# Kernel optimization log

Hardware: AMD Instinct MI355X
Metric: run time of the kernel (lower is better)

The kernel has to match this reference:

```python
import jax, jax.numpy as jnp
import numpy as np

B, C, D, H, W = 1, 32, 48, 96, 192


def setup_inputs() -> dict:
    key = jax.random.key(0)
    ks = jax.random.split(key, 5)
    x = jax.random.normal(ks[0], (B, C, D, H, W), dtype=jnp.float32)
    gs = []
    for i in range(4):
        g = jax.random.uniform(ks[i + 1], (B, C, 5, H, W), dtype=jnp.float32)
        # GANet normalizes the 5 aggregation weights to sum to 1 per pixel
        g = g / jnp.sum(g, axis=2, keepdims=True)
        gs.append(g)
    return {"input": x, "g0": gs[0], "g1": gs[1], "g2": gs[2], "g3": gs[3]}


def _sga_dir(cost, g, axis, reverse):
    """Semi-global aggregation along one direction.

    cost: (B,C,D,H,W); g: (B,C,5,H,W). axis=4 scans along width, axis=3 along
    height; reverse flips the scan direction. Recurrence per step p:
      A(p,d) = w0*C(p,d) + w1*A(p-1,d) + w2*A(p-1,d-1) + w3*A(p-1,d+1)
               + w4*max_d' A(p-1,d')
    with A = C at the first position and d+-1 edge-clamped.
    """
    c = jnp.moveaxis(cost, axis, 0)  # (L, B, C, D, R)
    w = jnp.moveaxis(g, axis, 0)     # (L, B, C, 5, R)
    if reverse:
        c = c[::-1]
        w = w[::-1]

    def step(A, xs):
        cs, ws = xs  # cs: (B,C,D,R); ws: (B,C,5,R)
        w0, w1, w2, w3, w4 = (ws[:, :, k][:, :, None] for k in range(5))
        dm1 = jnp.concatenate([A[:, :, :1], A[:, :, :-1]], axis=2)  # d-1 (clamped)
        dp1 = jnp.concatenate([A[:, :, 1:], A[:, :, -1:]], axis=2)  # d+1 (clamped)
        mx = jnp.max(A, axis=2, keepdims=True)                      # max over d
        A_new = w0 * cs + w1 * A + w2 * dm1 + w3 * dp1 + w4 * mx
        return A_new, A_new

    A0 = c[0]
    _, outs = jax.lax.scan(step, A0, (c[1:], w[1:]))
    full = jnp.concatenate([A0[None], outs], axis=0)
    if reverse:
        full = full[::-1]
    return jnp.moveaxis(full, 0, axis)


def reference(input, g0, g1, g2, g3):
    a0 = _sga_dir(input, g0, 4, False)  # left -> right
    a1 = _sga_dir(input, g1, 4, True)   # right -> left
    a2 = _sga_dir(input, g2, 3, False)  # top -> bottom
    a3 = _sga_dir(input, g3, 3, True)   # bottom -> top
    # GANet selects the max over the 4 directions instead of summing
    return jnp.maximum(jnp.maximum(a0, a1), jnp.maximum(a2, a3))
```

## Files before the change

kernel.cpp:

```cpp
#include <hip/hip_runtime.h>

constexpr int Cc = 32;
constexpr int Dd = 48;
constexpr int Hh = 96;
constexpr int Ww = 192;
constexpr int TW = 16;
constexpr int NT = Ww / TW;
constexpr float NEGBIG = -3.402823466e+38f;

template <int CTRL, int RM>
__device__ __forceinline__ float dppmov(float v) {
    int i = __builtin_bit_cast(int, v);
    int r = __builtin_amdgcn_update_dpp(i, i, CTRL, RM, 0xF, false);
    return __builtin_bit_cast(float, r);
}

__device__ __forceinline__ float rdlane(float v, int idx) {
    int r = __builtin_amdgcn_readlane(__builtin_bit_cast(int, v), idx);
    return __builtin_bit_cast(float, r);
}

__device__ __forceinline__ unsigned f2h(float v) {
    return (unsigned)__builtin_bit_cast(unsigned short, (_Float16)v);
}
__device__ __forceinline__ float h2f(unsigned short u) {
    return (float)__builtin_bit_cast(_Float16, u);
}

__device__ __forceinline__ float wave_max48(float v) {
    v = fmaxf(v, dppmov<0x111, 0xF>(v));
    v = fmaxf(v, dppmov<0x112, 0xF>(v));
    v = fmaxf(v, dppmov<0x114, 0xF>(v));
    v = fmaxf(v, dppmov<0x118, 0xF>(v));
    v = fmaxf(v, dppmov<0x142, 0x2>(v));
    v = fmaxf(v, dppmov<0x143, 0x4>(v));
    return rdlane(v, 47);
}

__device__ __forceinline__ float sga_step(float A, float cs, float g0v, float g1v, float g2v,
                                          float g3v, float g4v, bool is47, bool first) {
    float dm1 = dppmov<0x138, 0xF>(A);
    float dp1 = dppmov<0x130, 0xF>(A);
    dp1 = is47 ? A : dp1;
    float mx = wave_max48(A);
    float r = g0v * cs + g1v * A + g2v * dm1 + g3v * dp1 + g4v * mx;
    return first ? cs : r;
}

template <bool WS>
__global__ __launch_bounds__(64, 4) void sga_w4(const float* __restrict__ x,
                                                const float* __restrict__ ga,
                                                const float* __restrict__ gb,
                                                float* __restrict__ out,
                                                const unsigned* __restrict__ ws) {
    __shared__ unsigned sstash[64][Dd];
    __shared__ float xo[Dd][TW + 1];

    const int bid = blockIdx.x;
    const int c = bid / Hh;
    const int h = bid - c * Hh;
    const int lane = threadIdx.x;
    const size_t HW = (size_t)Hh * Ww;

    const float* xrow = x + (size_t)c * Dd * HW + (size_t)h * Ww;
    const float* garow = ga + (size_t)c * 5 * HW + (size_t)h * Ww;
    const float* gbrow = gb + (size_t)c * 5 * HW + (size_t)h * Ww;
    float* orow = out + (size_t)c * Dd * HW + (size_t)h * Ww;
    const size_t wsrow = ((size_t)c * Hh + h) * Dd;

    const int dl = (lane < Dd) ? lane : (Dd - 1);
    const bool is47 = (lane == Dd - 1);

    int srow[3], scol[3];
#pragma unroll
    for (int i = 0; i < 3; ++i) {
        const int e4 = lane + i * 64;
        srow[i] = e4 >> 2;
        scol[i] = (e4 & 3) * 4;
    }
    const int gk = lane >> 4;
    const int gwi = lane & 15;

    float4 pre[3];
    float gA, g4r, gAn = 0.f, g4n = 0.f;
    unsigned tr[8];
    unsigned sv0[8], sv1[8], sv2[8], sv3[8];

    {
#pragma unroll
        for (int i = 0; i < 3; ++i)
            pre[i] = *reinterpret_cast<const float4*>(xrow + (size_t)srow[i] * HW + scol[i]);
        gA = garow[(size_t)gk * HW + gwi];
        g4r = garow[(size_t)4 * HW + gwi];
#pragma unroll
        for (int i = 0; i < 3; ++i) {
            xo[srow[i]][scol[i] + 0] = pre[i].x;
            xo[srow[i]][scol[i] + 1] = pre[i].y;
            xo[srow[i]][scol[i] + 2] = pre[i].z;
            xo[srow[i]][scol[i] + 3] = pre[i].w;
        }
    }

    float A = NEGBIG;

    for (int t = 0; t < NT; ++t) {
        if (t + 1 < NT) {
            const int wn = (t + 1) * TW;
#pragma unroll
            for (int i = 0; i < 3; ++i)
                pre[i] = *reinterpret_cast<const float4*>(xrow + (size_t)srow[i] * HW + wn + scol[i]);
            gAn = garow[(size_t)gk * HW + wn + gwi];
            g4n = garow[(size_t)4 * HW + wn + gwi];
        }
#pragma unroll
        for (int wk = 0; wk < TW; ++wk) {
            const float g0v = rdlane(gA, wk);
            const float g1v = rdlane(gA, 16 + wk);
            const float g2v = rdlane(gA, 32 + wk);
            const float g3v = rdlane(gA, 48 + wk);
            const float g4v = rdlane(g4r, wk);
            const float cs = xo[dl][wk];
            A = sga_step(A, cs, g0v, g1v, g2v, g3v, g4v, is47, (t == 0 && wk == 0));
            const unsigned hu = f2h(A);
            if ((wk & 1) == 0) tr[wk >> 1] = hu;
            else tr[wk >> 1] |= hu << 16;
        }
        if (t < 8) {
            if (lane < Dd) {
#pragma unroll
                for (int r = 0; r < 8; ++r) sstash[t * 8 + r][lane] = tr[r];
            }
        } else if (t == 8) {
#pragma unroll
            for (int r = 0; r < 8; ++r) sv0[r] = tr[r];
        } else if (t == 9) {
#pragma unroll
            for (int r = 0; r < 8; ++r) sv1[r] = tr[r];
        } else if (t == 10) {
#pragma unroll
            for (int r = 0; r < 8; ++r) sv2[r] = tr[r];
        } else {
#pragma unroll
            for (int r = 0; r < 8; ++r) sv3[r] = tr[r];
        }
        if (t + 1 < NT) {
#pragma unroll
            for (int i = 0; i < 3; ++i) {
                xo[srow[i]][scol[i] + 0] = pre[i].x;
                xo[srow[i]][scol[i] + 1] = pre[i].y;
                xo[srow[i]][scol[i] + 2] = pre[i].z;
                xo[srow[i]][scol[i] + 3] = pre[i].w;
            }
            gA = gAn;
            g4r = g4n;
        }
    }

    A = NEGBIG;
    unsigned wsc[6], wsn[6];
    {
        const int w0 = (NT - 1) * TW;
        gA = gbrow[(size_t)gk * HW + w0 + gwi];
        g4r = gbrow[(size_t)4 * HW + w0 + gwi];
        if constexpr (WS) {
#pragma unroll
            for (int i = 0; i < 3; ++i) {
                const size_t wb = (wsrow + srow[i]) * 96 + (w0 >> 1) + (scol[i] >> 1);
                wsc[2 * i] = ws[wb];
                wsc[2 * i + 1] = ws[wb + 1];
            }
        }
    }
    for (int t = NT - 1; t >= 0; --t) {
        const int w0 = t * TW;
        if (t > 0) {
            const int wn = w0 - TW;
#pragma unroll
            for (int i = 0; i < 3; ++i)
                pre[i] = *reinterpret_cast<const float4*>(xrow + (size_t)srow[i] * HW + wn + scol[i]);
            gAn = gbrow[(size_t)gk * HW + wn + gwi];
            g4n = gbrow[(size_t)4 * HW + wn + gwi];
            if constexpr (WS) {
#pragma unroll
                for (int i = 0; i < 3; ++i) {
                    const size_t wb = (wsrow + srow[i]) * 96 + (wn >> 1) + (scol[i] >> 1);
                    wsn[2 * i] = ws[wb];
                    wsn[2 * i + 1] = ws[wb + 1];
                }
            }
        }
        unsigned rr[8];
        if (t < 8) {
#pragma unroll
            for (int r = 0; r < 8; ++r) rr[r] = sstash[t * 8 + r][dl];
        } else if (t == 8) {
#pragma unroll
            for (int r = 0; r < 8; ++r) rr[r] = sv0[r];
        } else if (t == 9) {
#pragma unroll
            for (int r = 0; r < 8; ++r) rr[r] = sv1[r];
        } else if (t == 10) {
#pragma unroll
            for (int r = 0; r < 8; ++r) rr[r] = sv2[r];
        } else {
#pragma unroll
            for (int r = 0; r < 8; ++r) rr[r] = sv3[r];
        }
#pragma unroll
        for (int wk = TW - 1; wk >= 0; --wk) {
            const float g0v = rdlane(gA, wk);
            const float g1v = rdlane(gA, 16 + wk);
            const float g2v = rdlane(gA, 32 + wk);
            const float g3v = rdlane(gA, 48 + wk);
            const float g4v = rdlane(g4r, wk);
            const float cs = xo[dl][wk];
            A = sga_step(A, cs, g0v, g1v, g2v, g3v, g4v, is47, (t == NT - 1 && wk == TW - 1));
            const unsigned u = rr[wk >> 1];
            const float a0 = h2f((unsigned short)((wk & 1) ? (u >> 16) : (u & 0xffffu)));
            if (lane < Dd) xo[lane][wk] = fmaxf(A, a0);
        }
#pragma unroll
        for (int i = 0; i < 3; ++i) {
            float4 v;
            v.x = xo[srow[i]][scol[i] + 0];
            v.y = xo[srow[i]][scol[i] + 1];
            v.z = xo[srow[i]][scol[i] + 2];
            v.w = xo[srow[i]][scol[i] + 3];
            if constexpr (WS) {
                v.x = fmaxf(v.x, h2f((unsigned short)(wsc[2 * i] & 0xffffu)));
                v.y = fmaxf(v.y, h2f((unsigned short)(wsc[2 * i] >> 16)));
                v.z = fmaxf(v.z, h2f((unsigned short)(wsc[2 * i + 1] & 0xffffu)));
                v.w = fmaxf(v.w, h2f((unsigned short)(wsc[2 * i + 1] >> 16)));
            }
            *reinterpret_cast<float4*>(orow + (size_t)srow[i] * HW + w0 + scol[i]) = v;
        }
        if (t > 0) {
#pragma unroll
            for (int i = 0; i < 3; ++i) {
                xo[srow[i]][scol[i] + 0] = pre[i].x;
                xo[srow[i]][scol[i] + 1] = pre[i].y;
                xo[srow[i]][scol[i] + 2] = pre[i].z;
                xo[srow[i]][scol[i] + 3] = pre[i].w;
            }
            gA = gAn;
            g4r = g4n;
            if constexpr (WS) {
#pragma unroll
                for (int i = 0; i < 6; ++i) wsc[i] = wsn[i];
            }
        }
    }
}

constexpr int WT2 = 4;
constexpr int KH2 = 2;
constexpr int NP2 = Hh / KH2;
constexpr int HALF2 = NP2 / 2;

template <bool WS>
__global__ __launch_bounds__(512, 2) void sga_h4(const float* __restrict__ x,
                                                 const float* __restrict__ gf,
                                                 const float* __restrict__ gr,
                                                 float* __restrict__ out,
                                                 unsigned* __restrict__ ws) {
    __shared__ unsigned short stash[WT2][2][Hh / 2][Dd];
    __shared__ float xs[2][2][KH2][Dd][WT2 + 1];
    __shared__ unsigned short osb[2][2][KH2][Dd][6];
    __shared__ float gs[2][2][KH2][WT2][8];

    const int xcd = blockIdx.x & 7;
    const int within = blockIdx.x >> 3;
    const int L = xcd * 192 + within;
    const int quad = L >> 2, sub = L & 3;
    const int c = quad / 12;
    const int wq = quad % 12;
    const int w0 = wq * 16 + sub * 4;

    const int tid = threadIdx.x;
    const int lane = tid & 63;
    const int wv = tid >> 6;
    const int col = wv >> 1;
    const int dir = wv & 1;
    const size_t HW = (size_t)Hh * Ww;

    const float* xb = x + (size_t)c * Dd * HW;
    const float* gfb = gf + (size_t)c * 5 * HW;
    const float* grb = gr + (size_t)c * 5 * HW;
    float* ob = out + (size_t)c * Dd * HW;

    const int dl = (lane < Dd) ? lane : (Dd - 1);
    const bool is47 = (lane == Dd - 1);

    int w_[2], d_[2], hp_[2], cu_[2];
    bool val_[2];
    size_t xoff_[2];
#pragma unroll
    for (int j = 0; j < 2; ++j) {
        int idx = tid + j * 512;
        val_[j] = idx < 768;
        if (idx >= 768) idx = 767;
        w_[j] = idx & 3;
        const int tt = idx >> 2;
        d_[j] = tt % Dd;
        const int t2 = tt / Dd;
        hp_[j] = t2 & 1;
        cu_[j] = t2 >> 1;
        xoff_[j] = (size_t)d_[j] * HW + (w0 + w_[j]);
    }
    const int gw_ = tid & 3;
    const int gk_ = (tid >> 2) % 5;
    const int ghc = (tid >> 2) / 5;
    const int ghp_ = ghc & 1;
    const int gcu_ = ghc >> 1;
    const bool gst = tid < 80;
    const int fwu = tid & 1;
    const int fd = (tid >> 1) % Dd;
    const int fr = (tid >> 1) / Dd;
    const int fhp = fr & 1;
    const int fcu = fr >> 1;
    const bool fval = tid < 384;

    auto hofs = [&](int cur, int P, int hp) -> int {
        const int p = P * KH2 + hp;
        return cur ? (Hh - 1 - p) : p;
    };

    float xr_[2], grg = 0.f;
    float orr[2][2];

    {
#pragma unroll
        for (int j = 0; j < 2; ++j)
            if (val_[j]) xr_[j] = xb[xoff_[j] + (size_t)hofs(cu_[j], 0, hp_[j]) * Ww];
        if (gst) {
            const float* gp = gcu_ ? grb : gfb;
            grg = gp[(size_t)gk_ * HW + (size_t)hofs(gcu_, 0, ghp_) * Ww + (w0 + gw_)];
        }
#pragma unroll
        for (int j = 0; j < 2; ++j)
            if (val_[j]) xs[0][cu_[j]][hp_[j]][d_[j]][w_[j]] = xr_[j];
        if (gst) gs[0][gcu_][ghp_][gw_][gk_] = grg;
    }
    __syncthreads();

    float A = NEGBIG;

#pragma unroll 2
    for (int p = 0; p < NP2; ++p) {
        const int pb = p & 1;

        if (p + 1 < NP2) {
#pragma unroll
            for (int j = 0; j < 2; ++j)
                if (val_[j]) xr_[j] = xb[xoff_[j] + (size_t)hofs(cu_[j], p + 1, hp_[j]) * Ww];
            if (gst) {
                const float* gp = gcu_ ? grb : gfb;
                grg = gp[(size_t)gk_ * HW + (size_t)hofs(gcu_, p + 1, ghp_) * Ww + (w0 + gw_)];
            }
        }
        if constexpr (!WS) {
            if (p >= HALF2) {
#pragma unroll
                for (int j = 0; j < 2; ++j)
                    if (val_[j]) orr[pb][j] = ob[xoff_[j] + (size_t)hofs(cu_[j], p, hp_[j]) * Ww];
            }
        }

#pragma unroll
        for (int hp = 0; hp < KH2; ++hp) {
            const int q = p * KH2 + hp;
            const float cs = xs[pb][dir][hp][dl][col];
            const float* gbase = &gs[pb][dir][hp][col][0];
            const float4 g03 = *reinterpret_cast<const float4*>(gbase);
            const float g4 = gbase[4];
            A = sga_step(A, cs, g03.x, g03.y, g03.z, g03.w, g4, is47, q == 0);
            if (q < Hh / 2) {
                if (lane < Dd) stash[col][dir][q][lane] = (unsigned short)f2h(A);
            } else {
                const float s = h2f(stash[col][dir ^ 1][Hh - 1 - q][dl]);
                const float o = fmaxf(A, s);
                if (lane < Dd) osb[pb][dir][hp][lane][col] = (unsigned short)f2h(o);
            }
        }

        if (p > HALF2) {
            if constexpr (WS) {
                if (fval) {
                    const unsigned* op = reinterpret_cast<const unsigned*>(&osb[pb ^ 1][fcu][fhp][fd][0]);
                    const unsigned v = op[fwu];
                    const int hh = hofs(fcu, p - 1, fhp);
                    ws[(((size_t)c * Hh + hh) * Dd + fd) * 96 + (w0 >> 1) + fwu] = v;
                }
            } else {
#pragma unroll
                for (int j = 0; j < 2; ++j) {
                    if (val_[j]) {
                        const float v = fmaxf(h2f(osb[pb ^ 1][cu_[j]][hp_[j]][d_[j]][w_[j]]),
                                              orr[pb ^ 1][j]);
                        ob[xoff_[j] + (size_t)hofs(cu_[j], p - 1, hp_[j]) * Ww] = v;
                    }
                }
            }
        }

        if (p + 1 < NP2) {
#pragma unroll
            for (int j = 0; j < 2; ++j)
                if (val_[j]) xs[pb ^ 1][cu_[j]][hp_[j]][d_[j]][w_[j]] = xr_[j];
            if (gst) gs[pb ^ 1][gcu_][ghp_][gw_][gk_] = grg;
        }
        __syncthreads();
    }

    if constexpr (WS) {
        if (fval) {
            const unsigned* op = reinterpret_cast<const unsigned*>(&osb[1][fcu][fhp][fd][0]);
            const unsigned v = op[fwu];
            const int hh = hofs(fcu, NP2 - 1, fhp);
            ws[(((size_t)c * Hh + hh) * Dd + fd) * 96 + (w0 >> 1) + fwu] = v;
        }
    } else {
#pragma unroll
        for (int j = 0; j < 2; ++j) {
            if (val_[j]) {
                const float v = fmaxf(h2f(osb[1][cu_[j]][hp_[j]][d_[j]][w_[j]]), orr[1][j]);
                ob[xoff_[j] + (size_t)hofs(cu_[j], NP2 - 1, hp_[j]) * Ww] = v;
            }
        }
    }
}

extern "C" void kernel_launch(void* const* d_in, const int* in_sizes, int n_in,
                              void* d_out, int out_size, void* d_ws, size_t ws_size,
                              hipStream_t stream) {
    const float* x  = (const float*)d_in[0];
    const float* g0 = (const float*)d_in[1];
    const float* g1 = (const float*)d_in[2];
    const float* g2 = (const float*)d_in[3];
    const float* g3 = (const float*)d_in[4];
    float* out = (float*)d_out;

    const size_t WSNEED = (size_t)Cc * Hh * Dd * Ww * 2;
    if (ws_size >= WSNEED) {
        sga_h4<true><<<Cc * (Ww / WT2), 512, 0, stream>>>(x, g2, g3, out, (unsigned*)d_ws);
        sga_w4<true><<<Cc * Hh, 64, 0, stream>>>(x, g0, g1, out, (const unsigned*)d_ws);
    } else {
        sga_w4<false><<<Cc * Hh, 64, 0, stream>>>(x, g0, g1, out, nullptr);
        sga_h4<false><<<Cc * (Ww / WT2), 512, 0, stream>>>(x, g2, g3, out, nullptr);
    }
}
```

Before: 289.8 us.

## Replace block-cooperative vertical scan with per-thread register scan over disparity

```diff
diff --git a/kernel.cpp b/kernel.cpp
--- a/kernel.cpp
+++ b/kernel.cpp
@@ -242,191 +242,127 @@
                 xo[srow[i]][scol[i] + 2] = pre[i].z;
                 xo[srow[i]][scol[i] + 3] = pre[i].w;
             }
+#pragma unroll
+            for (int i = 0; i < 6; ++i) wsc[i] = wsn[i];
             gA = gAn;
             g4r = g4n;
-            if constexpr (WS) {
-#pragma unroll
-                for (int i = 0; i < 6; ++i) wsc[i] = wsn[i];
-            }
-        }
-    }
-}
-
-constexpr int WT2 = 4;
-constexpr int KH2 = 2;
-constexpr int NP2 = Hh / KH2;
-constexpr int HALF2 = NP2 / 2;
-
-template <bool WS>
-__global__ __launch_bounds__(512, 2) void sga_h4(const float* __restrict__ x,
-                                                 const float* __restrict__ gf,
-                                                 const float* __restrict__ gr,
-                                                 float* __restrict__ out,
-                                                 unsigned* __restrict__ ws) {
-    __shared__ unsigned short stash[WT2][2][Hh / 2][Dd];
-    __shared__ float xs[2][2][KH2][Dd][WT2 + 1];
-    __shared__ unsigned short osb[2][2][KH2][Dd][6];
-    __shared__ float gs[2][2][KH2][WT2][8];
-
-    const int xcd = blockIdx.x & 7;
-    const int within = blockIdx.x >> 3;
-    const int L = xcd * 192 + within;
-    const int quad = L >> 2, sub = L & 3;
-    const int c = quad / 12;
-    const int wq = quad % 12;
-    const int w0 = wq * 16 + sub * 4;
-
-    const int tid = threadIdx.x;
-    const int lane = tid & 63;
-    const int wv = tid >> 6;
-    const int col = wv >> 1;
-    const int dir = wv & 1;
+        }
+    }
+}
+
+template <bool REV, int MODE>
+__global__ __launch_bounds__(64) void sga_hreg(const float* __restrict__ x,
+                                               const float* __restrict__ g,
+                                               unsigned short* __restrict__ ws,
+                                               float* __restrict__ out) {
+    const int c = blockIdx.x / 3;
+    const int w = (blockIdx.x % 3) * 64 + threadIdx.x;
     const size_t HW = (size_t)Hh * Ww;
 
     const float* xb = x + (size_t)c * Dd * HW;
-    const float* gfb = gf + (size_t)c * 5 * HW;
-    const float* grb = gr + (size_t)c * 5 * HW;
+    const float* gb = g + (size_t)c * 5 * HW;
+    unsigned short* wsb = ws + (size_t)c * Hh * Dd * Ww;
     float* ob = out + (size_t)c * Dd * HW;
 
-    const int dl = (lane < Dd) ? lane : (Dd - 1);
-    const bool is47 = (lane == Dd - 1);
-
-    int w_[2], d_[2], hp_[2], cu_[2];
-    bool val_[2];
-    size_t xoff_[2];
-#pragma unroll
-    for (int j = 0; j < 2; ++j) {
-        int idx = tid + j * 512;
-        val_[j] = idx < 768;
-        if (idx >= 768) idx = 767;
-        w_[j] = idx & 3;
-        const int tt = idx >> 2;
-        d_[j] = tt % Dd;
-        const int t2 = tt / Dd;
-        hp_[j] = t2 & 1;
-        cu_[j] = t2 >> 1;
-        xoff_[j] = (size_t)d_[j] * HW + (w0 + w_[j]);
-    }
-    const int gw_ = tid & 3;
-    const int gk_ = (tid >> 2) % 5;
-    const int ghc = (tid >> 2) / 5;
-    const int ghp_ = ghc & 1;
-    const int gcu_ = ghc >> 1;
-    const bool gst = tid < 80;
-    const int fwu = tid & 1;
-    const int fd = (tid >> 1) % Dd;
-    const int fr = (tid >> 1) / Dd;
-    const int fhp = fr & 1;
-    const int fcu = fr >> 1;
-    const bool fval = tid < 384;
-
-    auto hofs = [&](int cur, int P, int hp) -> int {
-        const int p = P * KH2 + hp;
-        return cur ? (Hh - 1 - p) : p;
-    };
-
-    float xr_[2], grg = 0.f;
-    float orr[2][2];
+    auto hof = [](int p) { return REV ? (Hh - 1 - p) : p; };
+
+    float A[Dd], xr[Dd], gr[5], gn[5];
+    unsigned short hl[Dd];
+    float wl[Dd];
 
     {
-#pragma unroll
-        for (int j = 0; j < 2; ++j)
-            if (val_[j]) xr_[j] = xb[xoff_[j] + (size_t)hofs(cu_[j], 0, hp_[j]) * Ww];
-        if (gst) {
-            const float* gp = gcu_ ? grb : gfb;
-            grg = gp[(size_t)gk_ * HW + (size_t)hofs(gcu_, 0, ghp_) * Ww + (w0 + gw_)];
-        }
-#pragma unroll
-        for (int j = 0; j < 2; ++j)
-            if (val_[j]) xs[0][cu_[j]][hp_[j]][d_[j]][w_[j]] = xr_[j];
-        if (gst) gs[0][gcu_][ghp_][gw_][gk_] = grg;
-    }
-    __syncthreads();
-
-    float A = NEGBIG;
-
-#pragma unroll 2
-    for (int p = 0; p < NP2; ++p) {
-        const int pb = p & 1;
-
-        if (p + 1 < NP2) {
-#pragma unroll
-            for (int j = 0; j < 2; ++j)
-                if (val_[j]) xr_[j] = xb[xoff_[j] + (size_t)hofs(cu_[j], p + 1, hp_[j]) * Ww];
-            if (gst) {
-                const float* gp = gcu_ ? grb : gfb;
-                grg = gp[(size_t)gk_ * HW + (size_t)hofs(gcu_, p + 1, ghp_) * Ww + (w0 + gw_)];
-            }
-        }
-        if constexpr (!WS) {
-            if (p >= HALF2) {
-#pragma unroll
-                for (int j = 0; j < 2; ++j)
-                    if (val_[j]) orr[pb][j] = ob[xoff_[j] + (size_t)hofs(cu_[j], p, hp_[j]) * Ww];
-            }
-        }
-
-#pragma unroll
-        for (int hp = 0; hp < KH2; ++hp) {
-            const int q = p * KH2 + hp;
-            const float cs = xs[pb][dir][hp][dl][col];
-            const float* gbase = &gs[pb][dir][hp][col][0];
-            const float4 g03 = *reinterpret_cast<const float4*>(gbase);
-            const float g4 = gbase[4];
-            A = sga_step(A, cs, g03.x, g03.y, g03.z, g03.w, g4, is47, q == 0);
-            if (q < Hh / 2) {
-                if (lane < Dd) stash[col][dir][q][lane] = (unsigned short)f2h(A);
-            } else {
-                const float s = h2f(stash[col][dir ^ 1][Hh - 1 - q][dl]);
-                const float o = fmaxf(A, s);
-                if (lane < Dd) osb[pb][dir][hp][lane][col] = (unsigned short)f2h(o);
-            }
-        }
-
-        if (p > HALF2) {
-            if constexpr (WS) {
-                if (fval) {
-                    const unsigned* op = reinterpret_cast<const unsigned*>(&osb[pb ^ 1][fcu][fhp][fd][0]);
-                    const unsigned v = op[fwu];
-                    const int hh = hofs(fcu, p - 1, fhp);
-                    ws[(((size_t)c * Hh + hh) * Dd + fd) * 96 + (w0 >> 1) + fwu] = v;
-                }
-            } else {
-#pragma unroll
-                for (int j = 0; j < 2; ++j) {
-                    if (val_[j]) {
-                        const float v = fmaxf(h2f(osb[pb ^ 1][cu_[j]][hp_[j]][d_[j]][w_[j]]),
-                                              orr[pb ^ 1][j]);
-                        ob[xoff_[j] + (size_t)hofs(cu_[j], p - 1, hp_[j]) * Ww] = v;
-                    }
-                }
-            }
-        }
-
-        if (p + 1 < NP2) {
-#pragma unroll
-            for (int j = 0; j < 2; ++j)
-                if (val_[j]) xs[pb ^ 1][cu_[j]][hp_[j]][d_[j]][w_[j]] = xr_[j];
-            if (gst) gs[pb ^ 1][gcu_][ghp_][gw_][gk_] = grg;
-        }
-        __syncthreads();
-    }
-
-    if constexpr (WS) {
-        if (fval) {
-            const unsigned* op = reinterpret_cast<const unsigned*>(&osb[1][fcu][fhp][fd][0]);
-            const unsigned v = op[fwu];
-            const int hh = hofs(fcu, NP2 - 1, fhp);
-            ws[(((size_t)c * Hh + hh) * Dd + fd) * 96 + (w0 >> 1) + fwu] = v;
-        }
-    } else {
-#pragma unroll
-        for (int j = 0; j < 2; ++j) {
-            if (val_[j]) {
-                const float v = fmaxf(h2f(osb[1][cu_[j]][hp_[j]][d_[j]][w_[j]]), orr[1][j]);
-                ob[xoff_[j] + (size_t)hofs(cu_[j], NP2 - 1, hp_[j]) * Ww] = v;
-            }
-        }
+        const int h0 = hof(0);
+#pragma unroll
+        for (int d = 0; d < Dd; ++d) xr[d] = xb[(size_t)d * HW + (size_t)h0 * Ww + w];
+        if (MODE == 1) {
+#pragma unroll
+            for (int d = 0; d < Dd; ++d) hl[d] = wsb[((size_t)h0 * Dd + d) * Ww + w];
+        } else if (MODE == 2) {
+#pragma unroll
+            for (int d = 0; d < Dd; ++d) wl[d] = ob[(size_t)d * HW + (size_t)h0 * Ww + w];
+        }
+        const int h1 = hof(1);
+#pragma unroll
+        for (int k = 0; k < 5; ++k) gr[k] = gb[(size_t)k * HW + (size_t)h1 * Ww + w];
+    }
+
+    {
+        const int h0 = hof(0);
+        const int h1 = hof(1);
+#pragma unroll
+        for (int d = 0; d < Dd; ++d) {
+            A[d] = xr[d];
+            if (MODE == 0)
+                wsb[((size_t)h0 * Dd + d) * Ww + w] = (unsigned short)f2h(A[d]);
+            xr[d] = xb[(size_t)d * HW + (size_t)h1 * Ww + w];
+        }
+    }
+
+    for (int p = 1; p < Hh; ++p) {
+        const int h = hof(p);
+        const int hn = hof(p + 1);
+        const bool notlast = (p + 1 < Hh);
+
+        if (notlast) {
+#pragma unroll
+            for (int k = 0; k < 5; ++k) gn[k] = gb[(size_t)k * HW + (size_t)hn * Ww + w];
+        }
+
+        if (MODE == 1) {
+            const int hm = hof(p - 1);
+#pragma unroll
+            for (int d = 0; d < Dd; ++d) {
+                const float m = fmaxf(A[d], h2f(hl[d]));
+                wsb[((size_t)hm * Dd + d) * Ww + w] = (unsigned short)f2h(m);
+                hl[d] = wsb[((size_t)h * Dd + d) * Ww + w];
+            }
+        } else if (MODE == 2) {
+            const int hm = hof(p - 1);
+#pragma unroll
+            for (int d = 0; d < Dd; ++d) {
+                ob[(size_t)d * HW + (size_t)hm * Ww + w] = fmaxf(A[d], wl[d]);
+                wl[d] = ob[(size_t)d * HW + (size_t)h * Ww + w];
+            }
+        }
+
+        float t0[24];
+#pragma unroll
+        for (int i = 0; i < 24; ++i) t0[i] = fmaxf(A[2 * i], A[2 * i + 1]);
+#pragma unroll
+        for (int i = 0; i < 12; ++i) t0[i] = fmaxf(t0[i], t0[i + 12]);
+#pragma unroll
+        for (int i = 0; i < 6; ++i) t0[i] = fmaxf(t0[i], t0[i + 6]);
+#pragma unroll
+        for (int i = 0; i < 3; ++i) t0[i] = fmaxf(t0[i], t0[i + 3]);
+        const float M = fmaxf(t0[0], fmaxf(t0[1], t0[2]));
+
+        float pm = A[0];
+#pragma unroll
+        for (int d = 0; d < Dd; ++d) {
+            const float cur = A[d];
+            const float np = (d < Dd - 1) ? A[d + 1] : cur;
+            A[d] = gr[0] * xr[d] + gr[1] * cur + gr[2] * pm + gr[3] * np + gr[4] * M;
+            pm = cur;
+            if (MODE == 0)
+                wsb[((size_t)h * Dd + d) * Ww + w] = (unsigned short)f2h(A[d]);
+            if (notlast) xr[d] = xb[(size_t)d * HW + (size_t)hn * Ww + w];
+        }
+#pragma unroll
+        for (int k = 0; k < 5; ++k) gr[k] = gn[k];
+    }
+
+    if (MODE == 1) {
+        const int hm = hof(Hh - 1);
+#pragma unroll
+        for (int d = 0; d < Dd; ++d) {
+            const float m = fmaxf(A[d], h2f(hl[d]));
+            wsb[((size_t)hm * Dd + d) * Ww + w] = (unsigned short)f2h(m);
+        }
+    } else if (MODE == 2) {
+        const int hm = hof(Hh - 1);
+#pragma unroll
+        for (int d = 0; d < Dd; ++d)
+            ob[(size_t)d * HW + (size_t)hm * Ww + w] = fmaxf(A[d], wl[d]);
     }
 }
 
@@ -442,10 +378,12 @@
 
     const size_t WSNEED = (size_t)Cc * Hh * Dd * Ww * 2;
     if (ws_size >= WSNEED) {
-        sga_h4<true><<<Cc * (Ww / WT2), 512, 0, stream>>>(x, g2, g3, out, (unsigned*)d_ws);
+        sga_hreg<false, 0><<<Cc * 3, 64, 0, stream>>>(x, g2, (unsigned short*)d_ws, out);
+        sga_hreg<true,  1><<<Cc * 3, 64, 0, stream>>>(x, g3, (unsigned short*)d_ws, out);
         sga_w4<true><<<Cc * Hh, 64, 0, stream>>>(x, g0, g1, out, (const unsigned*)d_ws);
     } else {
         sga_w4<false><<<Cc * Hh, 64, 0, stream>>>(x, g0, g1, out, nullptr);
-        sga_h4<false><<<Cc * (Ww / WT2), 512, 0, stream>>>(x, g2, g3, out, nullptr);
-    }
-}
+        sga_hreg<false, 2><<<Cc * 3, 64, 0, stream>>>(x, g2, nullptr, out);
+        sga_hreg<true,  2><<<Cc * 3, 64, 0, stream>>>(x, g3, nullptr, out);
+    }
+}
```

Result: slower. 569.1 us (+96.4%).
